# Kernel tuning notes

Measured on AMD Instinct MI355X. Metric: run time of the kernel, lower is better.

The kernel has to match this reference:

```python
import jax, jax.numpy as jnp
import numpy as np

MAX_WORDS = 256  # = batch['labels'].shape[1]


def _align(hidden, word_ids, max_words):
    """Batched segment-mean: (B,S,D) subtoken states -> (B,max_words,D) word states.
    Equivalent to align_subtokens_to_words applied per sample (word_ids all valid)."""
    B, S, D = hidden.shape
    seg = (word_ids.astype(jnp.int32) + jnp.arange(B, dtype=jnp.int32)[:, None] * max_words).reshape(-1)
    sums = jax.ops.segment_sum(hidden.reshape(-1, D), seg, num_segments=B * max_words)
    cnts = jax.ops.segment_sum(jnp.ones((B * S,), hidden.dtype), seg, num_segments=B * max_words)
    out = jnp.where(cnts[:, None] > 0, sums / jnp.maximum(cnts, 1.0)[:, None], 0.0)
    return out.reshape(B, max_words, D)


def setup_inputs() -> dict:
    key = jax.random.key(0)
    ks = jax.random.split(key, 8)
    B, S, D, W = 64, 512, 768, MAX_WORDS
    h_hing_sub = jax.random.normal(ks[0], (B, S, D), dtype=jnp.float32)
    h_rob_sub = jax.random.normal(ks[1], (B, S, D), dtype=jnp.float32)
    hing_word_ids = jnp.sort(jax.random.randint(ks[2], (B, S), 0, W), axis=-1).astype(jnp.int32)
    rob_word_ids = jnp.sort(jax.random.randint(ks[3], (B, S), 0, W), axis=-1).astype(jnp.int32)
    num_words = jax.random.randint(ks[4], (B,), 1, W).astype(jnp.int32)
    router_w1 = jax.random.normal(ks[5], (2 * D, 256), dtype=jnp.float32) * (1.0 / np.sqrt(2 * D))
    router_b1 = jnp.zeros((256,), jnp.float32)
    router_w2 = jax.random.normal(ks[6], (256, 1), dtype=jnp.float32) * (1.0 / 16.0)
    router_b2 = jnp.zeros((1,), jnp.float32)
    head_w = jax.random.normal(ks[7], (D, 7), dtype=jnp.float32) * (1.0 / np.sqrt(D))
    head_b = jnp.zeros((7,), jnp.float32)
    return {
        'h_hing_sub': h_hing_sub, 'h_rob_sub': h_rob_sub,
        'hing_word_ids': hing_word_ids, 'rob_word_ids': rob_word_ids,
        'num_words': num_words,
        'router_w1': router_w1, 'router_b1': router_b1,
        'router_w2': router_w2, 'router_b2': router_b2,
        'head_w': head_w, 'head_b': head_b,
    }


def reference(h_hing_sub, h_rob_sub, hing_word_ids, rob_word_ids, num_words,
              router_w1, router_b1, router_w2, router_b2, head_w, head_b):
    W = MAX_WORDS
    # scatter-mean subtokens -> words (the dominant custom-kernel op)
    h_hing = _align(h_hing_sub, hing_word_ids, W)   # (B, W, 768)
    h_rob = _align(h_rob_sub, rob_word_ids, W)      # (B, W, 768)
    # token-level MLP router on concatenated word states (router_input='both')
    router_in = jnp.concatenate([h_hing, h_rob], axis=-1)             # (B, W, 1536)
    hdn = jax.nn.relu(jnp.einsum('bwd,dh->bwh', router_in, router_w1) + router_b1)
    alpha = jax.nn.sigmoid(jnp.einsum('bwh,ho->bwo', hdn, router_w2) + router_b2)  # (B, W, 1)
    blended = alpha * h_hing + (1.0 - alpha) * h_rob                  # (B, W, 768)
    logits = jnp.einsum('bwd,dl->bwl', blended, head_w) + head_b      # (B, W, num_labels)
    l2_disagreement = jnp.linalg.norm(h_hing - h_rob, axis=-1)        # (B, W)
    return logits, alpha.squeeze(-1), l2_disagreement
```

## Files before the change

### kernel.cpp

```cpp
#include <hip/hip_runtime.h>
#include <hip/hip_bf16.h>
#include <math.h>

#define BATCH 64
#define SEQ   512
#define DIM   768
#define NW    256
#define NT    (BATCH * NW)
#define KDIM  1536
#define HID   256
#define NL    7

#define BM  32
#define BK  64
#define BKP 72
#define NKT (KDIM / BK)

typedef __bf16 bf16_t;
typedef bf16_t bf16x4 __attribute__((ext_vector_type(4)));
typedef bf16_t bf16x8 __attribute__((ext_vector_type(8)));
typedef float  f32x4  __attribute__((ext_vector_type(4)));

__device__ __forceinline__ void madv(f32x4& a, const f32x4& v, float s) {
    a[0] = fmaf(v[0], s, a[0]);
    a[1] = fmaf(v[1], s, a[1]);
    a[2] = fmaf(v[2], s, a[2]);
    a[3] = fmaf(v[3], s, a[3]);
}

__global__ __launch_bounds__(256) void convert_w1_kernel(
    const float* __restrict__ w1, bf16_t* __restrict__ w1t)
{
    int kc = blockIdx.x >> 3;
    int kg = blockIdx.x & 7;
    int n  = threadIdx.x;
    bf16x8 v;
    #pragma unroll
    for (int j = 0; j < 8; j++)
        v[j] = (bf16_t)w1[(size_t)(kc * 64 + kg * 8 + j) * HID + n];
    *(bf16x8*)(w1t + (size_t)kc * (HID * BK) + n * BK + kg * 8) = v;
}

__global__ __launch_bounds__(256) void starts_kernel(
    const int* __restrict__ idh, const int* __restrict__ idr,
    int* __restrict__ starts)
{
    int blk = blockIdx.x;
    int t = blk >> 6;
    int b = blk & 63;
    const int* ids = (t ? idr : idh) + b * SEQ;
    int w = threadIdx.x;
    int lo = 0, hi = SEQ;
    while (lo < hi) {
        int m = (lo + hi) >> 1;
        if (ids[m] < w) lo = m + 1; else hi = m;
    }
    int* row = starts + blk * 257;
    row[w] = lo;
    if (w == 0) row[256] = SEQ;
}

__global__ __launch_bounds__(256, 2) void align_kernel(
    const float* __restrict__ hh, const float* __restrict__ hr,
    const int* __restrict__ starts, bf16_t* __restrict__ X)
{
    int tid  = threadIdx.x;
    int lane = tid & 63;
    int wv   = tid >> 6;
    int task = blockIdx.x * 4 + wv;
    int b = task >> 7;
    int t = (task >> 6) & 1;
    int c = task & 63;
    int w0 = c * 4;

    const int*   st    = starts + (t * 64 + b) * 257;
    const f32x4* base4 = (const f32x4*)((t ? hr : hh) + (size_t)b * SEQ * DIM);
    bf16_t*      dstb  = X + (size_t)b * NW * KDIM + t * DIM;

    int lo = st[w0];
    #pragma unroll 1
    for (int w = w0; w < w0 + 4; w++) {
        int hi = st[w + 1];
        int ns = __builtin_amdgcn_readfirstlane(hi - lo);
        bf16_t* xr = dstb + (size_t)w * KDIM;

        if (ns <= 0) {
            bf16x4 z = {};
            *(bf16x4*)(xr + lane * 4)         = z;
            *(bf16x4*)(xr + (lane + 64) * 4)  = z;
            *(bf16x4*)(xr + (lane + 128) * 4) = z;
        } else {
            int nm1 = ns - 1;
            const f32x4* p0 = base4 + (size_t)lo * 192;
            const f32x4* p1 = base4 + (size_t)(lo + (1 < ns ? 1 : nm1)) * 192;
            const f32x4* p2 = base4 + (size_t)(lo + (2 < ns ? 2 : nm1)) * 192;
            const f32x4* p3 = base4 + (size_t)(lo + (3 < ns ? 3 : nm1)) * 192;
            const f32x4* p4 = base4 + (size_t)(lo + (4 < ns ? 4 : nm1)) * 192;
            const f32x4* p5 = base4 + (size_t)(lo + (5 < ns ? 5 : nm1)) * 192;

            f32x4 l0a = p0[lane], l0b = p0[lane + 64], l0c = p0[lane + 128];
            f32x4 l1a = p1[lane], l1b = p1[lane + 64], l1c = p1[lane + 128];
            f32x4 l2a = p2[lane], l2b = p2[lane + 64], l2c = p2[lane + 128];
            f32x4 l3a = p3[lane], l3b = p3[lane + 64], l3c = p3[lane + 128];
            f32x4 l4a = p4[lane], l4b = p4[lane + 64], l4c = p4[lane + 128];
            f32x4 l5a = p5[lane], l5b = p5[lane + 64], l5c = p5[lane + 128];

            float k1 = (1 < ns) ? 1.f : 0.f;
            float k2 = (2 < ns) ? 1.f : 0.f;
            float k3 = (3 < ns) ? 1.f : 0.f;
            float k4 = (4 < ns) ? 1.f : 0.f;
            float k5 = (5 < ns) ? 1.f : 0.f;

            f32x4 a0 = l0a, a1 = l0b, a2 = l0c;
            madv(a0, l1a, k1); madv(a1, l1b, k1); madv(a2, l1c, k1);
            madv(a0, l2a, k2); madv(a1, l2b, k2); madv(a2, l2c, k2);
            madv(a0, l3a, k3); madv(a1, l3b, k3); madv(a2, l3c, k3);
            madv(a0, l4a, k4); madv(a1, l4b, k4); madv(a2, l4c, k4);
            madv(a0, l5a, k5); madv(a1, l5b, k5); madv(a2, l5c, k5);

            if (ns > 6) {
                for (int s = lo + 6; s < lo + ns; s++) {
                    const f32x4* r = base4 + (size_t)s * 192;
                    a0 += r[lane]; a1 += r[lane + 64]; a2 += r[lane + 128];
                }
            }

            float inv = 1.0f / (float)ns;
            bf16x4 o0, o1, o2;
            #pragma unroll
            for (int e = 0; e < 4; e++) {
                o0[e] = (bf16_t)(a0[e] * inv);
                o1[e] = (bf16_t)(a1[e] * inv);
                o2[e] = (bf16_t)(a2[e] * inv);
            }
            *(bf16x4*)(xr + lane * 4)         = o0;
            *(bf16x4*)(xr + (lane + 64) * 4)  = o1;
            *(bf16x4*)(xr + (lane + 128) * 4) = o2;
        }
        lo = hi;
    }
}

__global__ __launch_bounds__(256) void gemm_alpha_kernel(
    const bf16_t* __restrict__ X, const bf16_t* __restrict__ w1t,
    const float* __restrict__ b1, const float* __restrict__ w2,
    const float* __restrict__ b2, float* __restrict__ out)
{
    __shared__ __align__(16) bf16_t Xs[BM][BKP];
    __shared__ __align__(16) bf16_t Ws[HID][BKP];
    __shared__ float alpha_acc[BM];

    int tid   = threadIdx.x;
    int lane  = tid & 63;
    int wv    = tid >> 6;
    int row16 = lane & 15;
    int quad  = lane >> 4;
    int tok0  = blockIdx.x * BM;

    f32x4 acc[2][4];
    #pragma unroll
    for (int mi = 0; mi < 2; mi++)
        #pragma unroll
        for (int ni = 0; ni < 4; ni++)
            acc[mi][ni] = (f32x4){0.f, 0.f, 0.f, 0.f};

    int xr = tid >> 3;
    int xc = tid & 7;

    for (int kc = 0; kc < NKT; kc++) {
        {
            const uint4* src = (const uint4*)(X + (size_t)(tok0 + xr) * KDIM + kc * BK + xc * 8);
            *(uint4*)(&Xs[xr][xc * 8]) = *src;
        }
        {
            const uint4* srcb = (const uint4*)(w1t + (size_t)kc * (HID * BK));
            #pragma unroll
            for (int i = 0; i < 8; i++) {
                int cidx = tid + i * 256;
                *(uint4*)(&Ws[cidx >> 3][(cidx & 7) * 8]) = srcb[cidx];
            }
        }
        __syncthreads();
        #pragma unroll
        for (int kk2 = 0; kk2 < 2; kk2++) {
            bf16x8 af[2], bfg[4];
            #pragma unroll
            for (int mi = 0; mi < 2; mi++)
                af[mi] = *(const bf16x8*)(&Xs[mi * 16 + row16][kk2 * 32 + quad * 8]);
            #pragma unroll
            for (int ni = 0; ni < 4; ni++)
                bfg[ni] = *(const bf16x8*)(&Ws[wv * 64 + ni * 16 + row16][kk2 * 32 + quad * 8]);
            #pragma unroll
            for (int mi = 0; mi < 2; mi++)
                #pragma unroll
                for (int ni = 0; ni < 4; ni++)
                    acc[mi][ni] = __builtin_amdgcn_mfma_f32_16x16x32_bf16(
                        af[mi], bfg[ni], acc[mi][ni], 0, 0, 0);
        }
        __syncthreads();
    }

    float w2v[4], b1v[4];
    #pragma unroll
    for (int ni = 0; ni < 4; ni++) {
        int col = wv * 64 + ni * 16 + row16;
        w2v[ni] = w2[col];
        b1v[ni] = b1[col];
    }
    if (tid < BM) alpha_acc[tid] = 0.f;
    __syncthreads();

    #pragma unroll
    for (int mi = 0; mi < 2; mi++) {
        #pragma unroll
        for (int r = 0; r < 4; r++) {
            float p = 0.f;
            #pragma unroll
            for (int ni = 0; ni < 4; ni++) {
                float v = acc[mi][ni][r] + b1v[ni];
                v = v > 0.f ? v : 0.f;
                p += v * w2v[ni];
            }
            p += __shfl_xor(p, 1);
            p += __shfl_xor(p, 2);
            p += __shfl_xor(p, 4);
            p += __shfl_xor(p, 8);
            if (row16 == 0)
                atomicAdd(&alpha_acc[mi * 16 + quad * 4 + r], p);
        }
    }
    __syncthreads();
    if (tid < BM) {
        float a = 1.f / (1.f + expf(-(alpha_acc[tid] + b2[0])));
        out[(size_t)NT * NL + tok0 + tid] = a;
    }
}

__global__ __launch_bounds__(256) void blend_kernel(
    const bf16_t* __restrict__ X, const float* __restrict__ hw,
    const float* __restrict__ hb, float* __restrict__ out)
{
    __shared__ float hws[NL * DIM];
    int tid  = threadIdx.x;
    int lane = tid & 63;
    int wv   = tid >> 6;

    for (int i = tid; i < DIM * NL; i += 256) {
        int d = i / NL, l = i - d * NL;
        hws[l * DIM + d] = hw[i];
    }
    __syncthreads();

    int g   = lane >> 3;
    int u   = lane & 7;
    int tok = blockIdx.x * 32 + wv * 8 + g;

    float a = out[(size_t)NT * NL + tok];
    const bf16_t* xrow = X + (size_t)tok * KDIM;

    float lg[NL] = {0.f, 0.f, 0.f, 0.f, 0.f, 0.f, 0.f};
    float l2 = 0.f;

    #pragma unroll
    for (int k = 0; k < 12; k++) {
        int d0 = (k * 8 + u) * 8;
        bf16x8 hp = *(const bf16x8*)(xrow + d0);
        bf16x8 rp = *(const bf16x8*)(xrow + DIM + d0);
        float bl[8];
        #pragma unroll
        for (int e = 0; e < 8; e++) {
            float hhv = (float)hp[e];
            float hrv = (float)rp[e];
            float df  = hhv - hrv;
            bl[e] = fmaf(a, df, hrv);
            l2 = fmaf(df, df, l2);
        }
        #pragma unroll
        for (int l = 0; l < NL; l++) {
            f32x4 wA = *(const f32x4*)(&hws[l * DIM + d0]);
            f32x4 wB = *(const f32x4*)(&hws[l * DIM + d0 + 4]);
            lg[l] += bl[0]*wA[0] + bl[1]*wA[1] + bl[2]*wA[2] + bl[3]*wA[3]
                   + bl[4]*wB[0] + bl[5]*wB[1] + bl[6]*wB[2] + bl[7]*wB[3];
        }
    }

    #pragma unroll
    for (int off = 1; off < 8; off <<= 1) {
        #pragma unroll
        for (int l = 0; l < NL; l++) lg[l] += __shfl_xor(lg[l], off);
        l2 += __shfl_xor(l2, off);
    }

    if (u < NL) {
        float v = (u == 0) ? lg[0] : (u == 1) ? lg[1] : (u == 2) ? lg[2]
                : (u == 3) ? lg[3] : (u == 4) ? lg[4] : (u == 5) ? lg[5] : lg[6];
        out[(size_t)tok * NL + u] = v + hb[u];
    } else {
        out[(size_t)NT * NL + NT + tok] = sqrtf(l2);
    }
}

extern "C" void kernel_launch(void* const* d_in, const int* in_sizes, int n_in,
                              void* d_out, int out_size, void* d_ws, size_t ws_size,
                              hipStream_t stream)
{
    const float* hh  = (const float*)d_in[0];
    const float* hr  = (const float*)d_in[1];
    const int*   idh = (const int*)d_in[2];
    const int*   idr = (const int*)d_in[3];
    const float* w1  = (const float*)d_in[5];
    const float* b1  = (const float*)d_in[6];
    const float* w2  = (const float*)d_in[7];
    const float* b2  = (const float*)d_in[8];
    const float* hw  = (const float*)d_in[9];
    const float* hb  = (const float*)d_in[10];
    float* out = (float*)d_out;

    bf16_t* X      = (bf16_t*)d_ws;
    bf16_t* w1t    = X + (size_t)NT * KDIM;
    int*    starts = (int*)(w1t + (size_t)NKT * HID * BK);

    convert_w1_kernel<<<192, 256, 0, stream>>>(w1, w1t);
    starts_kernel<<<128, 256, 0, stream>>>(idh, idr, starts);
    align_kernel<<<2048, 256, 0, stream>>>(hh, hr, starts, X);
    gemm_alpha_kernel<<<NT / BM, 256, 0, stream>>>(X, w1t, b1, w2, b2, out);
    blend_kernel<<<512, 256, 0, stream>>>(X, hw, hb, out);
}
```

Before: 289.5 us.

## Stream subtokens through double-buffered chunks in align kernel and merge prep kernels

The weight-conversion and segment-start kernels are merged into one prep launch, removing a kernel launch. The align kernel is restructured so each wavefront handles 16 words over a 256-float slice of the feature dimension. It streams that word range's subtoken rows in double-buffered chunks of 8 loads, emitting each word's mean when its boundary is crossed. The aim is to keep many independent loads in flight regardless of per-word subtoken counts, at the cost of clamped redundant loads in partial chunks and a more branchy drain loop.

```diff
diff --git a/kernel.cpp b/kernel.cpp
--- a/kernel.cpp
+++ b/kernel.cpp
@@ -21,44 +21,73 @@
 typedef bf16_t bf16x8 __attribute__((ext_vector_type(8)));
 typedef float  f32x4  __attribute__((ext_vector_type(4)));
 
-__device__ __forceinline__ void madv(f32x4& a, const f32x4& v, float s) {
-    a[0] = fmaf(v[0], s, a[0]);
-    a[1] = fmaf(v[1], s, a[1]);
-    a[2] = fmaf(v[2], s, a[2]);
-    a[3] = fmaf(v[3], s, a[3]);
-}
-
-__global__ __launch_bounds__(256) void convert_w1_kernel(
-    const float* __restrict__ w1, bf16_t* __restrict__ w1t)
-{
-    int kc = blockIdx.x >> 3;
-    int kg = blockIdx.x & 7;
-    int n  = threadIdx.x;
-    bf16x8 v;
-    #pragma unroll
-    for (int j = 0; j < 8; j++)
-        v[j] = (bf16_t)w1[(size_t)(kc * 64 + kg * 8 + j) * HID + n];
-    *(bf16x8*)(w1t + (size_t)kc * (HID * BK) + n * BK + kg * 8) = v;
-}
-
-__global__ __launch_bounds__(256) void starts_kernel(
+__global__ __launch_bounds__(256) void prep_kernel(
+    const float* __restrict__ w1, bf16_t* __restrict__ w1t,
     const int* __restrict__ idh, const int* __restrict__ idr,
     int* __restrict__ starts)
 {
-    int blk = blockIdx.x;
-    int t = blk >> 6;
-    int b = blk & 63;
-    const int* ids = (t ? idr : idh) + b * SEQ;
-    int w = threadIdx.x;
-    int lo = 0, hi = SEQ;
-    while (lo < hi) {
-        int m = (lo + hi) >> 1;
-        if (ids[m] < w) lo = m + 1; else hi = m;
-    }
-    int* row = starts + blk * 257;
-    row[w] = lo;
-    if (w == 0) row[256] = SEQ;
-}
+    if (blockIdx.x < 192) {
+        int kc = blockIdx.x >> 3;
+        int kg = blockIdx.x & 7;
+        int n  = threadIdx.x;
+        bf16x8 v;
+        #pragma unroll
+        for (int j = 0; j < 8; j++)
+            v[j] = (bf16_t)w1[(size_t)(kc * 64 + kg * 8 + j) * HID + n];
+        *(bf16x8*)(w1t + (size_t)kc * (HID * BK) + n * BK + kg * 8) = v;
+    } else {
+        int blk = blockIdx.x - 192;
+        int t = blk >> 6;
+        int b = blk & 63;
+        const int* ids = (t ? idr : idh) + b * SEQ;
+        int w = threadIdx.x;
+        int lo = 0, hi = SEQ;
+        while (lo < hi) {
+            int m = (lo + hi) >> 1;
+            if (ids[m] < w) lo = m + 1; else hi = m;
+        }
+        int* row = starts + blk * 257;
+        row[w] = lo;
+        if (w == 0) row[256] = SEQ;
+    }
+}
+
+#define WPT 16
+#define CH  8
+
+#define LOADCH(buf, cs_) {                                                    \
+    _Pragma("unroll")                                                         \
+    for (int i_ = 0; i_ < CH; i_++) {                                         \
+        int s_ = (cs_) + i_;                                                  \
+        s_ = s_ < hi ? s_ : hi - 1;                  \
+        buf[i_] = src[(size_t)s_ * 192 + lane];                               \
+    } }
+
+#define EMIT_ZERO(wid) *(bf16x4*)(dst + (size_t)(wid) * KDIM + lane * 4) = zero4;
+
+#define DRAIN(buf, cs_) {                                                     \
+    _Pragma("unroll")                                                         \
+    for (int i_ = 0; i_ < CH; i_++) {                                         \
+        int s_ = (cs_) + i_;                                                  \
+        if (s_ < hi) {                                                        \
+            acc[0] += buf[i_][0]; acc[1] += buf[i_][1];                       \
+            acc[2] += buf[i_][2]; acc[3] += buf[i_][3];                       \
+            if (s_ + 1 == nb) {                          \
+                float invn = 1.0f / (float)(nb - wstart);                     \
+                bf16x4 o;                                                     \
+                o[0] = (bf16_t)(acc[0] * invn); o[1] = (bf16_t)(acc[1] * invn);\
+                o[2] = (bf16_t)(acc[2] * invn); o[3] = (bf16_t)(acc[3] * invn);\
+                *(bf16x4*)(dst + (size_t)w * KDIM + lane * 4) = o;            \
+                acc = (f32x4){0.f, 0.f, 0.f, 0.f};                            \
+                w++; wstart = nb;                                             \
+                while (w < WPT) {                       \
+                    int nb2 = st[w + 1];                                      \
+                    if (nb2 > wstart) { nb = nb2; break; }                    \
+                    EMIT_ZERO(w); w++;                                        \
+                }                                                             \
+            }                                                                 \
+        }                                                                     \
+    } }
 
 __global__ __launch_bounds__(256, 2) void align_kernel(
     const float* __restrict__ hh, const float* __restrict__ hr,
@@ -68,76 +97,47 @@
     int lane = tid & 63;
     int wv   = tid >> 6;
     int task = blockIdx.x * 4 + wv;
-    int b = task >> 7;
-    int t = (task >> 6) & 1;
-    int c = task & 63;
-    int w0 = c * 4;
-
-    const int*   st    = starts + (t * 64 + b) * 257;
-    const f32x4* base4 = (const f32x4*)((t ? hr : hh) + (size_t)b * SEQ * DIM);
-    bf16_t*      dstb  = X + (size_t)b * NW * KDIM + t * DIM;
-
-    int lo = st[w0];
-    #pragma unroll 1
-    for (int w = w0; w < w0 + 4; w++) {
-        int hi = st[w + 1];
-        int ns = __builtin_amdgcn_readfirstlane(hi - lo);
-        bf16_t* xr = dstb + (size_t)w * KDIM;
-
-        if (ns <= 0) {
-            bf16x4 z = {};
-            *(bf16x4*)(xr + lane * 4)         = z;
-            *(bf16x4*)(xr + (lane + 64) * 4)  = z;
-            *(bf16x4*)(xr + (lane + 128) * 4) = z;
-        } else {
-            int nm1 = ns - 1;
-            const f32x4* p0 = base4 + (size_t)lo * 192;
-            const f32x4* p1 = base4 + (size_t)(lo + (1 < ns ? 1 : nm1)) * 192;
-            const f32x4* p2 = base4 + (size_t)(lo + (2 < ns ? 2 : nm1)) * 192;
-            const f32x4* p3 = base4 + (size_t)(lo + (3 < ns ? 3 : nm1)) * 192;
-            const f32x4* p4 = base4 + (size_t)(lo + (4 < ns ? 4 : nm1)) * 192;
-            const f32x4* p5 = base4 + (size_t)(lo + (5 < ns ? 5 : nm1)) * 192;
-
-            f32x4 l0a = p0[lane], l0b = p0[lane + 64], l0c = p0[lane + 128];
-            f32x4 l1a = p1[lane], l1b = p1[lane + 64], l1c = p1[lane + 128];
-            f32x4 l2a = p2[lane], l2b = p2[lane + 64], l2c = p2[lane + 128];
-            f32x4 l3a = p3[lane], l3b = p3[lane + 64], l3c = p3[lane + 128];
-            f32x4 l4a = p4[lane], l4b = p4[lane + 64], l4c = p4[lane + 128];
-            f32x4 l5a = p5[lane], l5b = p5[lane + 64], l5c = p5[lane + 128];
-
-            float k1 = (1 < ns) ? 1.f : 0.f;
-            float k2 = (2 < ns) ? 1.f : 0.f;
-            float k3 = (3 < ns) ? 1.f : 0.f;
-            float k4 = (4 < ns) ? 1.f : 0.f;
-            float k5 = (5 < ns) ? 1.f : 0.f;
-
-            f32x4 a0 = l0a, a1 = l0b, a2 = l0c;
-            madv(a0, l1a, k1); madv(a1, l1b, k1); madv(a2, l1c, k1);
-            madv(a0, l2a, k2); madv(a1, l2b, k2); madv(a2, l2c, k2);
-            madv(a0, l3a, k3); madv(a1, l3b, k3); madv(a2, l3c, k3);
-            madv(a0, l4a, k4); madv(a1, l4b, k4); madv(a2, l4c, k4);
-            madv(a0, l5a, k5); madv(a1, l5b, k5); madv(a2, l5c, k5);
-
-            if (ns > 6) {
-                for (int s = lo + 6; s < lo + ns; s++) {
-                    const f32x4* r = base4 + (size_t)s * 192;
-                    a0 += r[lane]; a1 += r[lane + 64]; a2 += r[lane + 128];
-                }
-            }
-
-            float inv = 1.0f / (float)ns;
-            bf16x4 o0, o1, o2;
-            #pragma unroll
-            for (int e = 0; e < 4; e++) {
-                o0[e] = (bf16_t)(a0[e] * inv);
-                o1[e] = (bf16_t)(a1[e] * inv);
-                o2[e] = (bf16_t)(a2[e] * inv);
-            }
-            *(bf16x4*)(xr + lane * 4)         = o0;
-            *(bf16x4*)(xr + (lane + 64) * 4)  = o1;
-            *(bf16x4*)(xr + (lane + 128) * 4) = o2;
-        }
-        lo = hi;
+    int dc   = task % 3;
+    int q    = task / 3;
+    int wb   = q & 15;
+    int t    = (q >> 4) & 1;
+    int b    = q >> 5;
+
+    const int*   st  = starts + (t * 64 + b) * 257 + wb * WPT;
+    const f32x4* src = (const f32x4*)((t ? hr : hh)
+                        + (size_t)b * SEQ * DIM + dc * 256);
+    bf16_t*      dst = X + (size_t)b * NW * KDIM + (size_t)wb * WPT * KDIM
+                         + t * DIM + dc * 256;
+
+    bf16x4 zero4 = {};
+    int lo = st[0];
+    int hi = st[WPT];
+
+    int w  = 0;
+    int nb = st[1];
+    while (nb == lo) {
+        EMIT_ZERO(w);
+        w++;
+        if (w == WPT) break;
+        nb = st[w + 1];
+    }
+
+    if (lo < hi) {
+        f32x4 acc = {0.f, 0.f, 0.f, 0.f};
+        int wstart = lo;
+        f32x4 bufA[CH], bufB[CH];
+        LOADCH(bufA, lo);
+        int cs = lo;
+        for (;;) {
+            LOADCH(bufB, cs + CH);
+            DRAIN(bufA, cs);
+            cs += CH;
+            if (cs >= hi) break;
+            LOADCH(bufA, cs + CH);
+            DRAIN(bufB, cs);
+            cs += CH;
+            if (cs >= hi) break;
+        }
     }
 }
 
@@ -320,9 +320,8 @@
     bf16_t* w1t    = X + (size_t)NT * KDIM;
     int*    starts = (int*)(w1t + (size_t)NKT * HID * BK);
 
-    convert_w1_kernel<<<192, 256, 0, stream>>>(w1, w1t);
-    starts_kernel<<<128, 256, 0, stream>>>(idh, idr, starts);
-    align_kernel<<<2048, 256, 0, stream>>>(hh, hr, starts, X);
+    prep_kernel<<<320, 256, 0, stream>>>(w1, w1t, idh, idr, starts);
+    align_kernel<<<1536, 256, 0, stream>>>(hh, hr, starts, X);
     gemm_alpha_kernel<<<NT / BM, 256, 0, stream>>>(X, w1t, b1, w2, b2, out);
     blend_kernel<<<512, 256, 0, stream>>>(X, hw, hb, out);
 }
```

Result: no change. 292.4 us (+1.0%).
